# Optimization experiments

Measured on AMD Instinct MI355X. Metric: run time of the kernel, lower is better.

## Reference

```python
import jax, jax.numpy as jnp
import numpy as np

B, IN, H = 131072, 128, 128


def setup_inputs() -> dict:
    key = jax.random.key(0)
    ks = jax.random.split(key, 8)
    scale_W = 1.0 / np.sqrt(IN + H)
    scale_r = 1.0 / np.sqrt(H)
    return {
        "x": jax.random.normal(ks[0], (B, IN), jnp.float32),
        "h": jax.random.normal(ks[1], (B, H), jnp.float32),
        "c": jax.random.normal(ks[2], (B, H), jnp.float32),
        "n": jax.random.uniform(ks[3], (B, H), jnp.float32, 0.1, 1.0),
        "m": jax.random.normal(ks[4], (B, H), jnp.float32),
        "W": jax.random.normal(ks[5], (IN + H, 4 * H), jnp.float32) * scale_W,
        "r": jax.random.normal(ks[6], (H, 4 * H), jnp.float32) * scale_r,
        "b": jnp.zeros((4 * H,), jnp.float32),
    }


def reference(x, h, c, n, m, W, r, b):
    # fused gate pre-activations: [B, 4H]
    combined = jnp.concatenate((x, h), axis=1)
    gates = combined @ W + h @ r + b
    i_raw, f_raw, z_raw, o_raw = jnp.split(gates, 4, axis=1)
    i = jnp.exp(i_raw)
    f = jax.nn.sigmoid(f_raw)
    z = jnp.tanh(z_raw)
    o = jax.nn.sigmoid(o_raw)
    # log-domain stabilizer (max trick), faithful to source incl. m overwrite
    m_new = jnp.maximum(jnp.log(f) + m, jnp.log(i))
    i_prime = jnp.exp(jnp.log(i) - m_new)
    f_prime = jnp.exp(jnp.log(f) + m_new - m_new)  # == f, as in source
    c_new = f_prime * c + i_prime * z
    n_new = f_prime * n + i_prime
    h_tilde = c_new / n_new
    h_new = o * jnp.tanh(h_tilde)
    return (h_new, c_new, n_new, m_new)
```

## Files before the change

### kernel.cpp

```cpp
#include <hip/hip_runtime.h>
#include <cstdint>

#define NROWS 131072
#define HD    128
#define NDIM  512
#define OUTQ  16777216

using bf16x8 = __attribute__((ext_vector_type(8))) short;
using f32x4  = __attribute__((ext_vector_type(4))) float;

#define SB() __builtin_amdgcn_sched_barrier(0)

__device__ __forceinline__ uint32_t bf16rne(float f) {
  uint32_t u = __builtin_bit_cast(uint32_t, f);
  return (u + 0x7fffu + ((u >> 16) & 1u)) >> 16;
}

__device__ __forceinline__ float tanhf_fast(float v) {
  float a = __builtin_fabsf(v);
  float e = __expf(-2.0f * a);
  float t = (1.0f - e) * __builtin_amdgcn_rcpf(1.0f + e);
  return v < 0.0f ? -t : t;
}

__device__ __forceinline__ f32x4 ldv(const float* p) {
  return *reinterpret_cast<const f32x4*>(p);
}

#define ASYNC16(g, l)                                                        \
  __builtin_amdgcn_global_load_lds(                                          \
      (const __attribute__((address_space(1))) void*)(g),                    \
      (__attribute__((address_space(3))) void*)(l), 16, 0, 0)

__global__ __launch_bounds__(256) void pack_weights(
    const float* __restrict__ W, const float* __restrict__ r,
    uint16_t* __restrict__ Bp) {
  int idx = blockIdx.x * 256 + threadIdx.x;
  int l  = idx & 63;
  int ts = idx >> 6;
  int s  = ts & 7;
  int t  = ts >> 3;
  int g  = t >> 3;
  int u  = t & 7;
  int t2 = u >> 1;
  int p  = u & 1;
  int m  = l & 15;
  int ncol  = g * 128 + t2 * 32 + ((m >> 2) << 3) + p * 4 + (m & 3);
  int kbase = s * 32 + ((l >> 4) << 3);
  uint32_t w[4];
#pragma unroll
  for (int jj = 0; jj < 4; ++jj) {
    int k0 = kbase + 2 * jj;
    float v0 = W[k0 * NDIM + ncol];
    float v1 = W[(k0 + 1) * NDIM + ncol];
    if (k0 >= 128)     v0 += r[(k0 - 128) * NDIM + ncol];
    if (k0 + 1 >= 128) v1 += r[(k0 + 1 - 128) * NDIM + ncol];
    w[jj] = bf16rne(v0) | (bf16rne(v1) << 16);
  }
  reinterpret_cast<uint4*>(Bp)[idx] = make_uint4(w[0], w[1], w[2], w[3]);
}

__global__ __launch_bounds__(256, 2) void slstm_fused(
    const float* __restrict__ x,  const float* __restrict__ h,
    const float* __restrict__ cs, const float* __restrict__ ns,
    const float* __restrict__ ms, const float* __restrict__ bias,
    const uint16_t* __restrict__ Bp, float* __restrict__ out) {
  __shared__ __align__(16) char smem[81920];
  const int tid  = threadIdx.x;
  const int wave = tid >> 6;
  const int lane = tid & 63;
  const int row0 = blockIdx.x * 64;
  const int l15  = lane & 15;
  const int lg   = lane >> 4;

  const int    myrow = row0 + wave * 16 + l15;
  const size_t rbase = (size_t)myrow * HD;
  const int    jb8   = lg * 8;
  const int    rl    = wave * 16 + l15;

  const char* wBytes = (const char*)Bp;
#define DMA_HALF(u, base)                                                    \
  {                                                                          \
    const char* gsrc = wBytes + (((size_t)(wave * 8 + (u)) * 8) << 10) + (lane << 4); \
    char* ldst = smem + (base) + (wave << 13);                               \
    _Pragma("unroll")                                                        \
    for (int k = 0; k < 8; ++k)                                              \
      ASYNC16(gsrc + (k << 10), ldst + (k << 10));                           \
  }

  f32x4 cvA = ldv(cs + rbase + jb8), cvHiA = ldv(cs + rbase + jb8 + 4);
  f32x4 nvA = ldv(ns + rbase + jb8), nvHiA = ldv(ns + rbase + jb8 + 4);
  f32x4 mvA = ldv(ms + rbase + jb8), mvHiA = ldv(ms + rbase + jb8 + 4);

  DMA_HALF(0, 0)
  DMA_HALF(1, 32768)

  bf16x8 a[8];
#pragma unroll
  for (int s = 0; s < 8; ++s) {
    const float* src = (s < 4 ? x : h) + rbase + ((s & 3) * 32 + lg * 8);
    f32x4 v0 = ldv(src);
    f32x4 v1 = ldv(src + 4);
    bf16x8 pk;
    pk[0] = (short)bf16rne(v0[0]);
    pk[1] = (short)bf16rne(v0[1]);
    pk[2] = (short)bf16rne(v0[2]);
    pk[3] = (short)bf16rne(v0[3]);
    pk[4] = (short)bf16rne(v1[0]);
    pk[5] = (short)bf16rne(v1[1]);
    pk[6] = (short)bf16rne(v1[2]);
    pk[7] = (short)bf16rne(v1[3]);
    a[s] = pk;
  }
  __syncthreads();

#define MFMA_PHASE(base, AI, AF, AZ, AO)                                     \
  {                                                                          \
    _Pragma("unroll")                                                        \
    for (int s = 0; s < 8; ++s) {                                            \
      const int lo = lane << 4;                                              \
      bf16x8 wI = *reinterpret_cast<const bf16x8*>(smem + (base) + ((0 * 8 + s) << 10) + lo); \
      bf16x8 wF = *reinterpret_cast<const bf16x8*>(smem + (base) + ((1 * 8 + s) << 10) + lo); \
      bf16x8 wZ = *reinterpret_cast<const bf16x8*>(smem + (base) + ((2 * 8 + s) << 10) + lo); \
      bf16x8 wO = *reinterpret_cast<const bf16x8*>(smem + (base) + ((3 * 8 + s) << 10) + lo); \
      AI = __builtin_amdgcn_mfma_f32_16x16x32_bf16(wI, a[s], AI, 0, 0, 0);   \
      AF = __builtin_amdgcn_mfma_f32_16x16x32_bf16(wF, a[s], AF, 0, 0, 0);   \
      AZ = __builtin_amdgcn_mfma_f32_16x16x32_bf16(wZ, a[s], AZ, 0, 0, 0);   \
      AO = __builtin_amdgcn_mfma_f32_16x16x32_bf16(wO, a[s], AO, 0, 0, 0);   \
    }                                                                        \
  }

  char* sbuf = smem + 65536;

#pragma unroll
  for (int t2 = 0; t2 < 4; ++t2) {
    const int cb = t2 * 32 + jb8;

    const f32x4 cvLo = cvA,   cvHi = cvHiA;
    const f32x4 nvLo = nvA,   nvHi = nvHiA;
    const f32x4 mvLo = mvA,   mvHi = mvHiA;

    SB(); asm volatile("s_waitcnt vmcnt(16)" ::: "memory"); SB();
    __builtin_amdgcn_s_barrier(); SB();

    f32x4 accI0 = {0,0,0,0}, accF0 = {0,0,0,0}, accZ0 = {0,0,0,0}, accO0 = {0,0,0,0};
    MFMA_PHASE(0, accI0, accF0, accZ0, accO0)

    SB(); asm volatile("s_waitcnt vmcnt(8)" ::: "memory"); SB();
    __builtin_amdgcn_s_barrier(); SB();

    const f32x4 bIlo = ldv(bias + cb),        bIhi = ldv(bias + cb + 4);
    const f32x4 bFlo = ldv(bias + 128 + cb),  bFhi = ldv(bias + 128 + cb + 4);
    const f32x4 bZlo = ldv(bias + 256 + cb),  bZhi = ldv(bias + 256 + cb + 4);
    const f32x4 bOlo = ldv(bias + 384 + cb),  bOhi = ldv(bias + 384 + cb + 4);
    if (t2 < 3) {
      const size_t pp = rbase + (t2 + 1) * 32 + jb8;
      cvA = ldv(cs + pp); cvHiA = ldv(cs + pp + 4);
      nvA = ldv(ns + pp); nvHiA = ldv(ns + pp + 4);
      mvA = ldv(ms + pp); mvHiA = ldv(ms + pp + 4);
    }

    f32x4 accI1 = {0,0,0,0}, accF1 = {0,0,0,0}, accZ1 = {0,0,0,0}, accO1 = {0,0,0,0};
    MFMA_PHASE(32768, accI1, accF1, accZ1, accO1)

    f32x4 hnLo, hnHi, cnLo, cnHi, nnLo, nnHi, mnLo, mnHi;
#pragma unroll
    for (int d = 0; d < 8; ++d) {
      const int pp = d >> 2, rr = d & 3;
      const float i_raw = (pp ? accI1[rr] : accI0[rr]) + (pp ? bIhi[rr] : bIlo[rr]);
      const float f_raw = (pp ? accF1[rr] : accF0[rr]) + (pp ? bFhi[rr] : bFlo[rr]);
      const float z_raw = (pp ? accZ1[rr] : accZ0[rr]) + (pp ? bZhi[rr] : bZlo[rr]);
      const float o_raw = (pp ? accO1[rr] : accO0[rr]) + (pp ? bOhi[rr] : bOlo[rr]);
      const float cV = pp ? cvHi[rr] : cvLo[rr];
      const float nV = pp ? nvHi[rr] : nvLo[rr];
      const float mV = pp ? mvHi[rr] : mvLo[rr];
      float ef  = __expf(-f_raw);
      float den = 1.0f + ef;
      float fg  = __builtin_amdgcn_rcpf(den);
      float lgf = -__logf(den);
      float mnv = fmaxf(lgf + mV, i_raw);
      float ip  = __expf(i_raw - mnv);
      float zt  = tanhf_fast(z_raw);
      float og  = __builtin_amdgcn_rcpf(1.0f + __expf(-o_raw));
      float cnv = fg * cV + ip * zt;
      float nnv = fg * nV + ip;
      float hnv = og * tanhf_fast(cnv * __builtin_amdgcn_rcpf(nnv));
      if (pp == 0) { hnLo[rr] = hnv; cnLo[rr] = cnv; nnLo[rr] = nnv; mnLo[rr] = mnv; }
      else         { hnHi[rr] = hnv; cnHi[rr] = cnv; nnHi[rr] = nnv; mnHi[rr] = mnv; }
    }

    const int rb   = rl << 7;
    const int sw   = rl & 7;
    const int oLo  = rb + ((((lg << 1)    ) ^ sw) << 4);
    const int oHi  = rb + ((((lg << 1) | 1) ^ sw) << 4);

    *reinterpret_cast<f32x4*>(sbuf + 0    + oLo) = hnLo;
    *reinterpret_cast<f32x4*>(sbuf + 0    + oHi) = hnHi;
    *reinterpret_cast<f32x4*>(sbuf + 8192 + oLo) = cnLo;
    *reinterpret_cast<f32x4*>(sbuf + 8192 + oHi) = cnHi;
    SB(); asm volatile("s_waitcnt lgkmcnt(0)" ::: "memory"); SB();
    __builtin_amdgcn_s_barrier(); SB();

    if (t2 < 3) {
      DMA_HALF(2 * t2 + 2, 0)
      DMA_HALF(2 * t2 + 3, 32768)
    }
    SB();

    {
      const int aw  = wave >> 1;
      const int rrb = (wave & 1) * 32;
      const char* sb = sbuf + aw * 8192;
      float* abase = out + (size_t)aw * OUTQ + (size_t)row0 * HD + t2 * 32;
#pragma unroll
      for (int i = 0; i < 4; ++i) {
        const int r = rrb + i * 8 + (lane >> 3);
        const int k = lane & 7;
        f32x4 v = *reinterpret_cast<const f32x4*>(
            sb + (r << 7) + (((k ^ (r & 7))) << 4));
        __builtin_nontemporal_store(
            v, reinterpret_cast<f32x4*>(abase + (size_t)r * HD + k * 4));
      }
    }
    SB(); asm volatile("s_waitcnt lgkmcnt(0)" ::: "memory"); SB();
    __builtin_amdgcn_s_barrier(); SB();

    *reinterpret_cast<f32x4*>(sbuf + 0    + oLo) = nnLo;
    *reinterpret_cast<f32x4*>(sbuf + 0    + oHi) = nnHi;
    *reinterpret_cast<f32x4*>(sbuf + 8192 + oLo) = mnLo;
    *reinterpret_cast<f32x4*>(sbuf + 8192 + oHi) = mnHi;
    SB(); asm volatile("s_waitcnt lgkmcnt(0)" ::: "memory"); SB();
    __builtin_amdgcn_s_barrier(); SB();

    {
      const int aw  = wave >> 1;
      const int rrb = (wave & 1) * 32;
      const char* sb = sbuf + aw * 8192;
      float* abase = out + (size_t)(2 + aw) * OUTQ + (size_t)row0 * HD + t2 * 32;
#pragma unroll
      for (int i = 0; i < 4; ++i) {
        const int r = rrb + i * 8 + (lane >> 3);
        const int k = lane & 7;
        f32x4 v = *reinterpret_cast<const f32x4*>(
            sb + (r << 7) + (((k ^ (r & 7))) << 4));
        __builtin_nontemporal_store(
            v, reinterpret_cast<f32x4*>(abase + (size_t)r * HD + k * 4));
      }
    }
  }
#undef DMA_HALF
#undef MFMA_PHASE
}

extern "C" void kernel_launch(void* const* d_in, const int* in_sizes, int n_in,
                              void* d_out, int out_size, void* d_ws, size_t ws_size,
                              hipStream_t stream) {
  const float* x = (const float*)d_in[0];
  const float* h = (const float*)d_in[1];
  const float* c = (const float*)d_in[2];
  const float* n = (const float*)d_in[3];
  const float* m = (const float*)d_in[4];
  const float* W = (const float*)d_in[5];
  const float* r = (const float*)d_in[6];
  const float* b = (const float*)d_in[7];
  uint16_t* Bp = (uint16_t*)d_ws;

  pack_weights<<<64, 256, 0, stream>>>(W, r, Bp);
  slstm_fused<<<NROWS / 64, 256, 0, stream>>>(x, h, c, n, m, b, Bp, (float*)d_out);
}
```

Before: 130.4 us.

## Double block to 128 rows with 8 waves and single-buffered weight staging

```diff
diff --git a/kernel.cpp b/kernel.cpp
--- a/kernel.cpp
+++ b/kernel.cpp
@@ -60,16 +60,16 @@
   reinterpret_cast<uint4*>(Bp)[idx] = make_uint4(w[0], w[1], w[2], w[3]);
 }
 
-__global__ __launch_bounds__(256, 2) void slstm_fused(
+__global__ __launch_bounds__(512, 4) void slstm_fused(
     const float* __restrict__ x,  const float* __restrict__ h,
     const float* __restrict__ cs, const float* __restrict__ ns,
     const float* __restrict__ ms, const float* __restrict__ bias,
     const uint16_t* __restrict__ Bp, float* __restrict__ out) {
-  __shared__ __align__(16) char smem[81920];
+  __shared__ __align__(16) char smem[65536];
   const int tid  = threadIdx.x;
   const int wave = tid >> 6;
   const int lane = tid & 63;
-  const int row0 = blockIdx.x * 64;
+  const int row0 = blockIdx.x * 128;
   const int l15  = lane & 15;
   const int lg   = lane >> 4;
 
@@ -79,12 +79,14 @@
   const int    rl    = wave * 16 + l15;
 
   const char* wBytes = (const char*)Bp;
-#define DMA_HALF(u, base)                                                    \
+  const int wg = wave >> 1;
+  const int ws = (wave & 1) * 4;
+#define DMA_HALF(u)                                                          \
   {                                                                          \
-    const char* gsrc = wBytes + (((size_t)(wave * 8 + (u)) * 8) << 10) + (lane << 4); \
-    char* ldst = smem + (base) + (wave << 13);                               \
+    const char* gsrc = wBytes + ((size_t)((wg * 8 + (u)) * 8 + ws) << 10) + (lane << 4); \
+    char* ldst = smem + ((wave * 4) << 10);                                  \
     _Pragma("unroll")                                                        \
-    for (int k = 0; k < 8; ++k)                                              \
+    for (int k = 0; k < 4; ++k)                                              \
       ASYNC16(gsrc + (k << 10), ldst + (k << 10));                           \
   }
 
@@ -92,8 +94,7 @@
   f32x4 nvA = ldv(ns + rbase + jb8), nvHiA = ldv(ns + rbase + jb8 + 4);
   f32x4 mvA = ldv(ms + rbase + jb8), mvHiA = ldv(ms + rbase + jb8 + 4);
 
-  DMA_HALF(0, 0)
-  DMA_HALF(1, 32768)
+  DMA_HALF(0)
 
   bf16x8 a[8];
 #pragma unroll
@@ -114,15 +115,15 @@
   }
   __syncthreads();
 
-#define MFMA_PHASE(base, AI, AF, AZ, AO)                                     \
+#define MFMA_PHASE(AI, AF, AZ, AO)                                           \
   {                                                                          \
     _Pragma("unroll")                                                        \
     for (int s = 0; s < 8; ++s) {                                            \
       const int lo = lane << 4;                                              \
-      bf16x8 wI = *reinterpret_cast<const bf16x8*>(smem + (base) + ((0 * 8 + s) << 10) + lo); \
-      bf16x8 wF = *reinterpret_cast<const bf16x8*>(smem + (base) + ((1 * 8 + s) << 10) + lo); \
-      bf16x8 wZ = *reinterpret_cast<const bf16x8*>(smem + (base) + ((2 * 8 + s) << 10) + lo); \
-      bf16x8 wO = *reinterpret_cast<const bf16x8*>(smem + (base) + ((3 * 8 + s) << 10) + lo); \
+      bf16x8 wI = *reinterpret_cast<const bf16x8*>(smem + ((0 * 8 + s) << 10) + lo); \
+      bf16x8 wF = *reinterpret_cast<const bf16x8*>(smem + ((1 * 8 + s) << 10) + lo); \
+      bf16x8 wZ = *reinterpret_cast<const bf16x8*>(smem + ((2 * 8 + s) << 10) + lo); \
+      bf16x8 wO = *reinterpret_cast<const bf16x8*>(smem + ((3 * 8 + s) << 10) + lo); \
       AI = __builtin_amdgcn_mfma_f32_16x16x32_bf16(wI, a[s], AI, 0, 0, 0);   \
       AF = __builtin_amdgcn_mfma_f32_16x16x32_bf16(wF, a[s], AF, 0, 0, 0);   \
       AZ = __builtin_amdgcn_mfma_f32_16x16x32_bf16(wZ, a[s], AZ, 0, 0, 0);   \
@@ -130,7 +131,7 @@
     }                                                                        \
   }
 
-  char* sbuf = smem + 65536;
+  char* sbuf = smem + 32768;
 
 #pragma unroll
   for (int t2 = 0; t2 < 4; ++t2) {
@@ -140,13 +141,16 @@
     const f32x4 nvLo = nvA,   nvHi = nvHiA;
     const f32x4 mvLo = mvA,   mvHi = mvHiA;
 
-    SB(); asm volatile("s_waitcnt vmcnt(16)" ::: "memory"); SB();
+    SB(); asm volatile("s_waitcnt vmcnt(8)" ::: "memory"); SB();
     __builtin_amdgcn_s_barrier(); SB();
 
     f32x4 accI0 = {0,0,0,0}, accF0 = {0,0,0,0}, accZ0 = {0,0,0,0}, accO0 = {0,0,0,0};
-    MFMA_PHASE(0, accI0, accF0, accZ0, accO0)
-
-    SB(); asm volatile("s_waitcnt vmcnt(8)" ::: "memory"); SB();
+    MFMA_PHASE(accI0, accF0, accZ0, accO0)
+
+    SB(); __builtin_amdgcn_s_barrier(); SB();
+    DMA_HALF(2 * t2 + 1)
+    SB();
+    asm volatile("s_waitcnt vmcnt(0)" ::: "memory"); SB();
     __builtin_amdgcn_s_barrier(); SB();
 
     const f32x4 bIlo = ldv(bias + cb),        bIhi = ldv(bias + cb + 4);
@@ -161,7 +165,7 @@
     }
 
     f32x4 accI1 = {0,0,0,0}, accF1 = {0,0,0,0}, accZ1 = {0,0,0,0}, accO1 = {0,0,0,0};
-    MFMA_PHASE(32768, accI1, accF1, accZ1, accO1)
+    MFMA_PHASE(accI1, accF1, accZ1, accO1)
 
     f32x4 hnLo, hnHi, cnLo, cnHi, nnLo, nnHi, mnLo, mnHi;
 #pragma unroll
@@ -194,23 +198,20 @@
     const int oLo  = rb + ((((lg << 1)    ) ^ sw) << 4);
     const int oHi  = rb + ((((lg << 1) | 1) ^ sw) << 4);
 
-    *reinterpret_cast<f32x4*>(sbuf + 0    + oLo) = hnLo;
-    *reinterpret_cast<f32x4*>(sbuf + 0    + oHi) = hnHi;
-    *reinterpret_cast<f32x4*>(sbuf + 8192 + oLo) = cnLo;
-    *reinterpret_cast<f32x4*>(sbuf + 8192 + oHi) = cnHi;
+    *reinterpret_cast<f32x4*>(sbuf + 0     + oLo) = hnLo;
+    *reinterpret_cast<f32x4*>(sbuf + 0     + oHi) = hnHi;
+    *reinterpret_cast<f32x4*>(sbuf + 16384 + oLo) = cnLo;
+    *reinterpret_cast<f32x4*>(sbuf + 16384 + oHi) = cnHi;
     SB(); asm volatile("s_waitcnt lgkmcnt(0)" ::: "memory"); SB();
     __builtin_amdgcn_s_barrier(); SB();
 
-    if (t2 < 3) {
-      DMA_HALF(2 * t2 + 2, 0)
-      DMA_HALF(2 * t2 + 3, 32768)
-    }
+    if (t2 < 3) DMA_HALF(2 * t2 + 2)
     SB();
 
     {
-      const int aw  = wave >> 1;
-      const int rrb = (wave & 1) * 32;
-      const char* sb = sbuf + aw * 8192;
+      const int aw  = wave >> 2;
+      const int rrb = (wave & 3) * 32;
+      const char* sb = sbuf + aw * 16384;
       float* abase = out + (size_t)aw * OUTQ + (size_t)row0 * HD + t2 * 32;
 #pragma unroll
       for (int i = 0; i < 4; ++i) {
@@ -225,17 +226,17 @@
     SB(); asm volatile("s_waitcnt lgkmcnt(0)" ::: "memory"); SB();
     __builtin_amdgcn_s_barrier(); SB();
 
-    *reinterpret_cast<f32x4*>(sbuf + 0    + oLo) = nnLo;
-    *reinterpret_cast<f32x4*>(sbuf + 0    + oHi) = nnHi;
-    *reinterpret_cast<f32x4*>(sbuf + 8192 + oLo) = mnLo;
-    *reinterpret_cast<f32x4*>(sbuf + 8192 + oHi) = mnHi;
+    *reinterpret_cast<f32x4*>(sbuf + 0     + oLo) = nnLo;
+    *reinterpret_cast<f32x4*>(sbuf + 0     + oHi) = nnHi;
+    *reinterpret_cast<f32x4*>(sbuf + 16384 + oLo) = mnLo;
+    *reinterpret_cast<f32x4*>(sbuf + 16384 + oHi) = mnHi;
     SB(); asm volatile("s_waitcnt lgkmcnt(0)" ::: "memory"); SB();
     __builtin_amdgcn_s_barrier(); SB();
 
     {
-      const int aw  = wave >> 1;
-      const int rrb = (wave & 1) * 32;
-      const char* sb = sbuf + aw * 8192;
+      const int aw  = wave >> 2;
+      const int rrb = (wave & 3) * 32;
+      const char* sb = sbuf + aw * 16384;
       float* abase = out + (size_t)(2 + aw) * OUTQ + (size_t)row0 * HD + t2 * 32;
 #pragma unroll
       for (int i = 0; i < 4; ++i) {
@@ -266,5 +267,5 @@
   uint16_t* Bp = (uint16_t*)d_ws;
 
   pack_weights<<<64, 256, 0, stream>>>(W, r, Bp);
-  slstm_fused<<<NROWS / 64, 256, 0, stream>>>(x, h, c, n, m, b, Bp, (float*)d_out);
-}
+  slstm_fused<<<NROWS / 128, 512, 0, stream>>>(x, h, c, n, m, b, Bp, (float*)d_out);
+}
```

After: 244.7 us. 87.6% more time.

## Load packed weights directly from global into MFMA operands, dropping LDS staging

Applied to the files above, without the earlier changes.

```diff
diff --git a/kernel.cpp b/kernel.cpp
--- a/kernel.cpp
+++ b/kernel.cpp
@@ -26,11 +26,6 @@
 __device__ __forceinline__ f32x4 ldv(const float* p) {
   return *reinterpret_cast<const f32x4*>(p);
 }
-
-#define ASYNC16(g, l)                                                        \
-  __builtin_amdgcn_global_load_lds(                                          \
-      (const __attribute__((address_space(1))) void*)(g),                    \
-      (__attribute__((address_space(3))) void*)(l), 16, 0, 0)
 
 __global__ __launch_bounds__(256) void pack_weights(
     const float* __restrict__ W, const float* __restrict__ r,
@@ -65,7 +60,7 @@
     const float* __restrict__ cs, const float* __restrict__ ns,
     const float* __restrict__ ms, const float* __restrict__ bias,
     const uint16_t* __restrict__ Bp, float* __restrict__ out) {
-  __shared__ __align__(16) char smem[81920];
+  __shared__ __align__(16) char sbuf[16384];
   const int tid  = threadIdx.x;
   const int wave = tid >> 6;
   const int lane = tid & 63;
@@ -78,22 +73,9 @@
   const int    jb8   = lg * 8;
   const int    rl    = wave * 16 + l15;
 
-  const char* wBytes = (const char*)Bp;
-#define DMA_HALF(u, base)                                                    \
-  {                                                                          \
-    const char* gsrc = wBytes + (((size_t)(wave * 8 + (u)) * 8) << 10) + (lane << 4); \
-    char* ldst = smem + (base) + (wave << 13);                               \
-    _Pragma("unroll")                                                        \
-    for (int k = 0; k < 8; ++k)                                              \
-      ASYNC16(gsrc + (k << 10), ldst + (k << 10));                           \
-  }
-
   f32x4 cvA = ldv(cs + rbase + jb8), cvHiA = ldv(cs + rbase + jb8 + 4);
   f32x4 nvA = ldv(ns + rbase + jb8), nvHiA = ldv(ns + rbase + jb8 + 4);
   f32x4 mvA = ldv(ms + rbase + jb8), mvHiA = ldv(ms + rbase + jb8 + 4);
-
-  DMA_HALF(0, 0)
-  DMA_HALF(1, 32768)
 
   bf16x8 a[8];
 #pragma unroll
@@ -112,25 +94,8 @@
     pk[7] = (short)bf16rne(v1[3]);
     a[s] = pk;
   }
-  __syncthreads();
-
-#define MFMA_PHASE(base, AI, AF, AZ, AO)                                     \
-  {                                                                          \
-    _Pragma("unroll")                                                        \
-    for (int s = 0; s < 8; ++s) {                                            \
-      const int lo = lane << 4;                                              \
-      bf16x8 wI = *reinterpret_cast<const bf16x8*>(smem + (base) + ((0 * 8 + s) << 10) + lo); \
-      bf16x8 wF = *reinterpret_cast<const bf16x8*>(smem + (base) + ((1 * 8 + s) << 10) + lo); \
-      bf16x8 wZ = *reinterpret_cast<const bf16x8*>(smem + (base) + ((2 * 8 + s) << 10) + lo); \
-      bf16x8 wO = *reinterpret_cast<const bf16x8*>(smem + (base) + ((3 * 8 + s) << 10) + lo); \
-      AI = __builtin_amdgcn_mfma_f32_16x16x32_bf16(wI, a[s], AI, 0, 0, 0);   \
-      AF = __builtin_amdgcn_mfma_f32_16x16x32_bf16(wF, a[s], AF, 0, 0, 0);   \
-      AZ = __builtin_amdgcn_mfma_f32_16x16x32_bf16(wZ, a[s], AZ, 0, 0, 0);   \
-      AO = __builtin_amdgcn_mfma_f32_16x16x32_bf16(wO, a[s], AO, 0, 0, 0);   \
-    }                                                                        \
-  }
-
-  char* sbuf = smem + 65536;
+
+  const bf16x8* __restrict__ Bf = reinterpret_cast<const bf16x8*>(Bp);
 
 #pragma unroll
   for (int t2 = 0; t2 < 4; ++t2) {
@@ -140,13 +105,7 @@
     const f32x4 nvLo = nvA,   nvHi = nvHiA;
     const f32x4 mvLo = mvA,   mvHi = mvHiA;
 
-    SB(); asm volatile("s_waitcnt vmcnt(16)" ::: "memory"); SB();
-    __builtin_amdgcn_s_barrier(); SB();
-
-    f32x4 accI0 = {0,0,0,0}, accF0 = {0,0,0,0}, accZ0 = {0,0,0,0}, accO0 = {0,0,0,0};
-    MFMA_PHASE(0, accI0, accF0, accZ0, accO0)
-
-    SB(); asm volatile("s_waitcnt vmcnt(8)" ::: "memory"); SB();
+    SB(); asm volatile("s_waitcnt lgkmcnt(0)" ::: "memory"); SB();
     __builtin_amdgcn_s_barrier(); SB();
 
     const f32x4 bIlo = ldv(bias + cb),        bIhi = ldv(bias + cb + 4);
@@ -160,8 +119,23 @@
       mvA = ldv(ms + pp); mvHiA = ldv(ms + pp + 4);
     }
 
+    const int u0 = 2 * t2, u1 = u0 + 1;
+    f32x4 accI0 = {0,0,0,0}, accF0 = {0,0,0,0}, accZ0 = {0,0,0,0}, accO0 = {0,0,0,0};
+#pragma unroll
+    for (int s = 0; s < 8; ++s) {
+      accI0 = __builtin_amdgcn_mfma_f32_16x16x32_bf16(Bf[(size_t)(((0 * 8 + u0) * 8) + s) * 64 + lane], a[s], accI0, 0, 0, 0);
+      accF0 = __builtin_amdgcn_mfma_f32_16x16x32_bf16(Bf[(size_t)(((1 * 8 + u0) * 8) + s) * 64 + lane], a[s], accF0, 0, 0, 0);
+      accZ0 = __builtin_amdgcn_mfma_f32_16x16x32_bf16(Bf[(size_t)(((2 * 8 + u0) * 8) + s) * 64 + lane], a[s], accZ0, 0, 0, 0);
+      accO0 = __builtin_amdgcn_mfma_f32_16x16x32_bf16(Bf[(size_t)(((3 * 8 + u0) * 8) + s) * 64 + lane], a[s], accO0, 0, 0, 0);
+    }
     f32x4 accI1 = {0,0,0,0}, accF1 = {0,0,0,0}, accZ1 = {0,0,0,0}, accO1 = {0,0,0,0};
-    MFMA_PHASE(32768, accI1, accF1, accZ1, accO1)
+#pragma unroll
+    for (int s = 0; s < 8; ++s) {
+      accI1 = __builtin_amdgcn_mfma_f32_16x16x32_bf16(Bf[(size_t)(((0 * 8 + u1) * 8) + s) * 64 + lane], a[s], accI1, 0, 0, 0);
+      accF1 = __builtin_amdgcn_mfma_f32_16x16x32_bf16(Bf[(size_t)(((1 * 8 + u1) * 8) + s) * 64 + lane], a[s], accF1, 0, 0, 0);
+      accZ1 = __builtin_amdgcn_mfma_f32_16x16x32_bf16(Bf[(size_t)(((2 * 8 + u1) * 8) + s) * 64 + lane], a[s], accZ1, 0, 0, 0);
+      accO1 = __builtin_amdgcn_mfma_f32_16x16x32_bf16(Bf[(size_t)(((3 * 8 + u1) * 8) + s) * 64 + lane], a[s], accO1, 0, 0, 0);
+    }
 
     f32x4 hnLo, hnHi, cnLo, cnHi, nnLo, nnHi, mnLo, mnHi;
 #pragma unroll
@@ -201,12 +175,6 @@
     SB(); asm volatile("s_waitcnt lgkmcnt(0)" ::: "memory"); SB();
     __builtin_amdgcn_s_barrier(); SB();
 
-    if (t2 < 3) {
-      DMA_HALF(2 * t2 + 2, 0)
-      DMA_HALF(2 * t2 + 3, 32768)
-    }
-    SB();
-
     {
       const int aw  = wave >> 1;
       const int rrb = (wave & 1) * 32;
@@ -248,8 +216,6 @@
       }
     }
   }
-#undef DMA_HALF
-#undef MFMA_PHASE
 }
 
 extern "C" void kernel_launch(void* const* d_in, const int* in_sizes, int n_in,
```

New measurement: 162.1 us. 1.24x slower.
